# Kernel tuning notes

Measured on AMD Instinct MI355X. Metric: run time of the kernel, lower is better.

## Reference

```python
import jax, jax.numpy as jnp
import numpy as np


def setup_inputs() -> dict:
    key = jax.random.key(0)
    B, N, D = 32, 1024, 1024
    x = jax.random.normal(key, (B, N, D), dtype=jnp.float32)
    return {"x": x}


def reference(x) -> jnp.ndarray:
    # query = key = value = x (the module's Linear layers are unused).
    # kl_divs[b,i,j] = KL(softmax(x[b,i]) || softmax(x[b,j])) for i != j, 0 on diag.
    # Since KL(p||p) == 0, the full vectorized KL matrix matches the looped version.
    logp = jax.nn.log_softmax(x, axis=-1)          # [B, N, D]
    p = jnp.exp(logp)                               # softmax(x)
    neg_ent = jnp.sum(p * logp, axis=-1)            # [B, N]  = sum p log p
    cross = jnp.einsum('bid,bjd->bij', p, logp)     # [B, N, N] = sum_d p_i log q_j
    kl = neg_ent[:, :, None] - cross                # [B, N, N]
    attn = jax.nn.softmax(-kl, axis=-1)             # [B, N, N]
    out = jnp.einsum('bij,bjd->bid', attn, x)       # value = x
    return out
```

## Files before the change

### kernel.cpp

```cpp
#include <hip/hip_runtime.h>
#include <hip/hip_bf16.h>
#include <stdint.h>

#define B_ 32
#define N_ 1024
#define D_ 1024

typedef __bf16 bf16x8 __attribute__((ext_vector_type(8)));
typedef float f32x4 __attribute__((ext_vector_type(4)));

static __device__ __forceinline__ unsigned short f2bf(float f) {
    union { float f; unsigned u; } v; v.f = f;
    unsigned r = v.u + 0x7fffu + ((v.u >> 16) & 1u);
    return (unsigned short)(r >> 16);
}

static __device__ __forceinline__ void gld_lds16(const void* g, void* l) {
    __builtin_amdgcn_global_load_lds(
        (const __attribute__((address_space(1))) void*)g,
        (__attribute__((address_space(3))) void*)l, 16, 0, 0);
}

__global__ __launch_bounds__(256) void prep_kernel(const float* __restrict__ x,
        unsigned short* __restrict__ pb, unsigned short* __restrict__ xb,
        float* __restrict__ lse) {
    int row  = blockIdx.x * 4 + (threadIdx.x >> 6);
    int lane = threadIdx.x & 63;
    const float4* xr = (const float4*)(x + (size_t)row * D_);

    float4 v[4];
    #pragma unroll
    for (int q = 0; q < 4; q++) v[q] = xr[lane + 64 * q];

    float m = -1e30f;
    #pragma unroll
    for (int q = 0; q < 4; q++)
        m = fmaxf(m, fmaxf(fmaxf(v[q].x, v[q].y), fmaxf(v[q].z, v[q].w)));
    #pragma unroll
    for (int o = 1; o < 64; o <<= 1) m = fmaxf(m, __shfl_xor(m, o, 64));

    float4 e[4];
    float s = 0.0f;
    #pragma unroll
    for (int q = 0; q < 4; q++) {
        e[q].x = __expf(v[q].x - m); e[q].y = __expf(v[q].y - m);
        e[q].z = __expf(v[q].z - m); e[q].w = __expf(v[q].w - m);
        s += e[q].x + e[q].y + e[q].z + e[q].w;
    }
    #pragma unroll
    for (int o = 1; o < 64; o <<= 1) s += __shfl_xor(s, o, 64);
    float inv = 1.0f / s;

    ushort4* pr = (ushort4*)(pb + (size_t)row * D_);
    ushort4* xw = (ushort4*)(xb + (size_t)row * D_);
    #pragma unroll
    for (int q = 0; q < 4; q++) {
        ushort4 pu, xu;
        pu.x = f2bf(e[q].x * inv); pu.y = f2bf(e[q].y * inv);
        pu.z = f2bf(e[q].z * inv); pu.w = f2bf(e[q].w * inv);
        xu.x = f2bf(v[q].x); xu.y = f2bf(v[q].y);
        xu.z = f2bf(v[q].z); xu.w = f2bf(v[q].w);
        pr[lane + 64 * q] = pu;
        xw[lane + 64 * q] = xu;
    }
    if (lane == 0) lse[row] = m + logf(s);
}

template<int MODE>
__global__ __launch_bounds__(256) void gemm_bt(const unsigned short* __restrict__ Ag,
        const unsigned short* __restrict__ Bg, void* __restrict__ Cg,
        const float* __restrict__ lse, float* __restrict__ rowsum) {
    const int K = 1024;
    int b = blockIdx.z;
    const unsigned short* A  = Ag + (size_t)b * N_ * K;
    const unsigned short* Bm = Bg + (size_t)b * N_ * K;
    int m0 = blockIdx.y * 128, n0 = blockIdx.x * 128;

    __shared__ unsigned short lds[2][128 * 32];
    int t = threadIdx.x;
    int wave = t >> 6, lane = t & 63;
    int wr = wave >> 1, wc = wave & 1;

    f32x4 acc[4][4];
    #pragma unroll
    for (int i = 0; i < 4; i++)
        #pragma unroll
        for (int j = 0; j < 4; j++)
            #pragma unroll
            for (int r = 0; r < 4; r++) acc[i][j][r] = 0.0f;

    int fm = lane & 15;
    int gf = lane >> 4;

    for (int k0 = 0; k0 < K; k0 += 32) {
        __syncthreads();
        #pragma unroll
        for (int h = 0; h < 2; h++) {
            int c = h * 256 + t;
            int r = c >> 2;
            int g = (c & 3) ^ ((r >> 1) & 3);
            gld_lds16(A  + (size_t)(m0 + r) * K + k0 + g * 8, (char*)&lds[0][0] + c * 16);
            gld_lds16(Bm + (size_t)(n0 + r) * K + k0 + g * 8, (char*)&lds[1][0] + c * 16);
        }
        __syncthreads();

        bf16x8 av[4], bv[4];
        #pragma unroll
        for (int i = 0; i < 4; i++) {
            int ra = wr * 64 + i * 16 + fm;
            int rb = wc * 64 + i * 16 + fm;
            av[i] = *(const bf16x8*)&lds[0][ra * 32 + ((gf ^ ((ra >> 1) & 3)) * 8)];
            bv[i] = *(const bf16x8*)&lds[1][rb * 32 + ((gf ^ ((rb >> 1) & 3)) * 8)];
        }
        #pragma unroll
        for (int i = 0; i < 4; i++)
            #pragma unroll
            for (int j = 0; j < 4; j++)
                acc[i][j] = __builtin_amdgcn_mfma_f32_16x16x32_bf16(av[i], bv[j], acc[i][j], 0, 0, 0);
    }

    int cr = (lane >> 4) * 4;
    int cc = lane & 15;

    if (MODE == 0) {
        unsigned short* Co = (unsigned short*)Cg + (size_t)b * (size_t)N_ * N_;
        float lsev[4];
        #pragma unroll
        for (int j = 0; j < 4; j++) lsev[j] = lse[b * N_ + n0 + wc * 64 + j * 16 + cc];
        float rsum[16];
        #pragma unroll
        for (int q = 0; q < 16; q++) rsum[q] = 0.0f;
        #pragma unroll
        for (int i = 0; i < 4; i++) {
            #pragma unroll
            for (int r = 0; r < 4; r++) {
                int row = m0 + wr * 64 + i * 16 + cr + r;
                size_t ro = (size_t)row * N_;
                #pragma unroll
                for (int j = 0; j < 4; j++) {
                    int col = n0 + wc * 64 + j * 16 + cc;
                    float ev = __expf(acc[i][j][r] - lsev[j]);
                    unsigned short eb = f2bf(ev);
                    union { unsigned u; float f; } bk; bk.u = ((unsigned)eb) << 16;
                    Co[ro + col] = eb;
                    rsum[i * 4 + r] += bk.f;
                }
            }
        }
        #pragma unroll
        for (int q = 0; q < 16; q++) {
            float sv = rsum[q];
            sv += __shfl_xor(sv, 1, 64);
            sv += __shfl_xor(sv, 2, 64);
            sv += __shfl_xor(sv, 4, 64);
            sv += __shfl_xor(sv, 8, 64);
            rsum[q] = sv;
        }
        if (cc == 0) {
            #pragma unroll
            for (int q = 0; q < 16; q++) {
                int row = m0 + wr * 64 + (q >> 2) * 16 + cr + (q & 3);
                atomicAdd(&rowsum[b * N_ + row], rsum[q]);
            }
        }
    } else {
        float* Co = (float*)Cg + (size_t)b * (size_t)N_ * N_;
        #pragma unroll
        for (int i = 0; i < 4; i++) {
            #pragma unroll
            for (int r = 0; r < 4; r++) {
                int row = m0 + wr * 64 + i * 16 + cr + r;
                float inv = 1.0f / rowsum[b * N_ + row];
                size_t ro = (size_t)row * N_;
                #pragma unroll
                for (int j = 0; j < 4; j++) {
                    int col = n0 + wc * 64 + j * 16 + cc;
                    Co[ro + col] = acc[i][j][r] * inv;
                }
            }
        }
    }
}

__global__ __launch_bounds__(256) void transpose_kernel(const unsigned short* __restrict__ in,
        unsigned short* __restrict__ out) {
    int b  = blockIdx.z;
    int j0 = blockIdx.y * 64;
    int d0 = blockIdx.x * 64;
    __shared__ unsigned short tile[64][66];
    const unsigned short* ip = in + ((size_t)b * N_ + j0) * D_ + d0;
    int t = threadIdx.x;
    #pragma unroll
    for (int c = t; c < 512; c += 256) {
        int r = c >> 3, col = (c & 7) * 8;
        uint4 val = *(const uint4*)(ip + (size_t)r * D_ + col);
        unsigned int* dst = (unsigned int*)&tile[r][col];
        dst[0] = val.x; dst[1] = val.y; dst[2] = val.z; dst[3] = val.w;
    }
    __syncthreads();
    unsigned short* op = out + ((size_t)b * D_ + d0) * N_ + j0;
    #pragma unroll
    for (int c = t; c < 512; c += 256) {
        int r = c >> 3, col = (c & 7) * 8;
        unsigned short vals[8];
        #pragma unroll
        for (int k = 0; k < 8; k++) vals[k] = tile[col + k][r];
        uint4 o;
        o.x = (unsigned)vals[0] | ((unsigned)vals[1] << 16);
        o.y = (unsigned)vals[2] | ((unsigned)vals[3] << 16);
        o.z = (unsigned)vals[4] | ((unsigned)vals[5] << 16);
        o.w = (unsigned)vals[6] | ((unsigned)vals[7] << 16);
        *(uint4*)(op + (size_t)r * N_ + col) = o;
    }
}

extern "C" void kernel_launch(void* const* d_in, const int* in_sizes, int n_in,
                              void* d_out, int out_size, void* d_ws, size_t ws_size,
                              hipStream_t stream) {
    const float* x = (const float*)d_in[0];
    float* out = (float*)d_out;
    char* ws = (char*)d_ws;

    unsigned short* pb    = (unsigned short*)(ws);
    unsigned short* xb    = (unsigned short*)(ws + 67108864ULL);
    unsigned short* xbT   = (unsigned short*)(ws + 134217728ULL);
    unsigned short* attnE = (unsigned short*)(ws + 201326592ULL);
    float*          lse   = (float*)(ws + 268435456ULL);
    float*          rowsum= (float*)(ws + 268566528ULL);

    hipMemsetAsync(rowsum, 0, B_ * N_ * sizeof(float), stream);
    prep_kernel<<<dim3(B_ * N_ / 4), 256, 0, stream>>>(x, pb, xb, lse);
    transpose_kernel<<<dim3(16, 16, B_), 256, 0, stream>>>(xb, xbT);
    gemm_bt<0><<<dim3(8, 8, B_), 256, 0, stream>>>(pb, xb, attnE, lse, rowsum);
    gemm_bt<1><<<dim3(8, 8, B_), 256, 0, stream>>>(attnE, xbT, out, nullptr, rowsum);
}
```

Baseline: 480.1 us.

## Enlarge GEMM tiles to 256x256 with double-buffered async LDS pipeline

Both batched GEMMs now use 256x256 output tiles with 512 threads (8 waves, 2x4 layout). Each wave computes 128x64 in two halves. K-tiles are double-buffered in LDS, and direct global-to-LDS loads are issued up to three stages ahead, with explicit vmcnt waits, barriers and s_setprio around the MFMA blocks. The goal is more data reuse per LDS byte and loads hidden behind compute. In exchange it uses more registers and 64KB of LDS, and the grid shrinks to 512 blocks, which may lower occupancy.

```diff
diff --git a/kernel.cpp b/kernel.cpp
--- a/kernel.cpp
+++ b/kernel.cpp
@@ -67,56 +67,88 @@
 }
 
 template<int MODE>
-__global__ __launch_bounds__(256) void gemm_bt(const unsigned short* __restrict__ Ag,
+__global__ __launch_bounds__(512) void gemm_bt(const unsigned short* __restrict__ Ag,
         const unsigned short* __restrict__ Bg, void* __restrict__ Cg,
         const float* __restrict__ lse, float* __restrict__ rowsum) {
     const int K = 1024;
     int b = blockIdx.z;
     const unsigned short* A  = Ag + (size_t)b * N_ * K;
     const unsigned short* Bm = Bg + (size_t)b * N_ * K;
-    int m0 = blockIdx.y * 128, n0 = blockIdx.x * 128;
-
-    __shared__ unsigned short lds[2][128 * 32];
+    int m0 = blockIdx.y * 256, n0 = blockIdx.x * 256;
+
+    __shared__ unsigned short lds[32768];
+
     int t = threadIdx.x;
     int wave = t >> 6, lane = t & 63;
-    int wr = wave >> 1, wc = wave & 1;
-
-    f32x4 acc[4][4];
-    #pragma unroll
-    for (int i = 0; i < 4; i++)
+    int wr = wave >> 2, wc = wave & 3;
+    int fm = lane & 15, gf = lane >> 4;
+    int rsw = (fm >> 1) & 3;
+
+    f32x4 acc[8][4];
+    #pragma unroll
+    for (int i = 0; i < 8; i++)
         #pragma unroll
         for (int j = 0; j < 4; j++)
             #pragma unroll
             for (int r = 0; r < 4; r++) acc[i][j][r] = 0.0f;
 
-    int fm = lane & 15;
-    int gf = lane >> 4;
-
-    for (int k0 = 0; k0 < K; k0 += 32) {
-        __syncthreads();
-        #pragma unroll
-        for (int h = 0; h < 2; h++) {
-            int c = h * 256 + t;
-            int r = c >> 2;
-            int g = (c & 3) ^ ((r >> 1) & 3);
-            gld_lds16(A  + (size_t)(m0 + r) * K + k0 + g * 8, (char*)&lds[0][0] + c * 16);
-            gld_lds16(Bm + (size_t)(n0 + r) * K + k0 + g * 8, (char*)&lds[1][0] + c * 16);
-        }
-        __syncthreads();
-
-        bf16x8 av[4], bv[4];
-        #pragma unroll
-        for (int i = 0; i < 4; i++) {
-            int ra = wr * 64 + i * 16 + fm;
-            int rb = wc * 64 + i * 16 + fm;
-            av[i] = *(const bf16x8*)&lds[0][ra * 32 + ((gf ^ ((ra >> 1) & 3)) * 8)];
-            bv[i] = *(const bf16x8*)&lds[1][rb * 32 + ((gf ^ ((rb >> 1) & 3)) * 8)];
-        }
-        #pragma unroll
-        for (int i = 0; i < 4; i++)
-            #pragma unroll
-            for (int j = 0; j < 4; j++)
-                acc[i][j] = __builtin_amdgcn_mfma_f32_16x16x32_bf16(av[i], bv[j], acc[i][j], 0, 0, 0);
+    int rr = t >> 2, s = t & 3;
+    int sg = s ^ ((rr >> 1) & 3);
+    int rbase = rr + (rr & 64);
+
+    auto stage = [&](int g) {
+        int tg = g >> 1, qg = g & 1, bg = tg & 1;
+        int row = qg * 64 + rbase;
+        const unsigned short* sa = A  + (size_t)(m0 + row) * K + tg * 32 + sg * 8;
+        const unsigned short* sb = Bm + (size_t)(n0 + row) * K + tg * 32 + sg * 8;
+        gld_lds16(sa, &lds[bg * 8192 + row * 32 + s * 8]);
+        gld_lds16(sb, &lds[16384 + bg * 8192 + row * 32 + s * 8]);
+    };
+
+    stage(0); stage(1); stage(2);
+    asm volatile("s_waitcnt vmcnt(2)" ::: "memory");
+    __builtin_amdgcn_s_barrier();
+
+    for (int tt = 0; tt < 32; ++tt) {
+        int bb = tt & 1;
+        const unsigned short* LA = &lds[bb * 8192];
+        const unsigned short* LB = &lds[16384 + bb * 8192];
+        bf16x8 bv[4];
+        #pragma unroll
+        for (int q = 0; q < 2; ++q) {
+            if (q == 0) {
+                #pragma unroll
+                for (int j = 0; j < 4; ++j) {
+                    int row = wc * 64 + j * 16 + fm;
+                    bv[j] = *(const bf16x8*)&LB[row * 32 + (gf ^ rsw) * 8];
+                }
+            }
+            bf16x8 av[4];
+            #pragma unroll
+            for (int i2 = 0; i2 < 4; ++i2) {
+                int row = wr * 128 + (q * 4 + i2) * 16 + fm;
+                av[i2] = *(const bf16x8*)&LA[row * 32 + (gf ^ rsw) * 8];
+            }
+            int g = 2 * tt + q + 3;
+            if (g < 64) stage(g);
+
+            __builtin_amdgcn_s_barrier();
+            asm volatile("s_waitcnt lgkmcnt(0)" ::: "memory");
+            __builtin_amdgcn_sched_barrier(0);
+            __builtin_amdgcn_s_setprio(1);
+            #pragma unroll
+            for (int i2 = 0; i2 < 4; ++i2)
+                #pragma unroll
+                for (int j = 0; j < 4; ++j)
+                    acc[q * 4 + i2][j] = __builtin_amdgcn_mfma_f32_16x16x32_bf16(
+                        av[i2], bv[j], acc[q * 4 + i2][j], 0, 0, 0);
+            __builtin_amdgcn_s_setprio(0);
+            if (q == 1) {
+                if (tt < 30)       asm volatile("s_waitcnt vmcnt(2)" ::: "memory");
+                else if (tt == 30) asm volatile("s_waitcnt vmcnt(0)" ::: "memory");
+            }
+            __builtin_amdgcn_s_barrier();
+        }
     }
 
     int cr = (lane >> 4) * 4;
@@ -127,14 +159,14 @@
         float lsev[4];
         #pragma unroll
         for (int j = 0; j < 4; j++) lsev[j] = lse[b * N_ + n0 + wc * 64 + j * 16 + cc];
-        float rsum[16];
-        #pragma unroll
-        for (int q = 0; q < 16; q++) rsum[q] = 0.0f;
-        #pragma unroll
-        for (int i = 0; i < 4; i++) {
+        float rsum[32];
+        #pragma unroll
+        for (int q = 0; q < 32; q++) rsum[q] = 0.0f;
+        #pragma unroll
+        for (int i = 0; i < 8; i++) {
             #pragma unroll
             for (int r = 0; r < 4; r++) {
-                int row = m0 + wr * 64 + i * 16 + cr + r;
+                int row = m0 + wr * 128 + i * 16 + cr + r;
                 size_t ro = (size_t)row * N_;
                 #pragma unroll
                 for (int j = 0; j < 4; j++) {
@@ -148,7 +180,7 @@
             }
         }
         #pragma unroll
-        for (int q = 0; q < 16; q++) {
+        for (int q = 0; q < 32; q++) {
             float sv = rsum[q];
             sv += __shfl_xor(sv, 1, 64);
             sv += __shfl_xor(sv, 2, 64);
@@ -158,18 +190,18 @@
         }
         if (cc == 0) {
             #pragma unroll
-            for (int q = 0; q < 16; q++) {
-                int row = m0 + wr * 64 + (q >> 2) * 16 + cr + (q & 3);
+            for (int q = 0; q < 32; q++) {
+                int row = m0 + wr * 128 + (q >> 2) * 16 + cr + (q & 3);
                 atomicAdd(&rowsum[b * N_ + row], rsum[q]);
             }
         }
     } else {
         float* Co = (float*)Cg + (size_t)b * (size_t)N_ * N_;
         #pragma unroll
-        for (int i = 0; i < 4; i++) {
+        for (int i = 0; i < 8; i++) {
             #pragma unroll
             for (int r = 0; r < 4; r++) {
-                int row = m0 + wr * 64 + i * 16 + cr + r;
+                int row = m0 + wr * 128 + i * 16 + cr + r;
                 float inv = 1.0f / rowsum[b * N_ + row];
                 size_t ro = (size_t)row * N_;
                 #pragma unroll
@@ -231,6 +263,6 @@
     hipMemsetAsync(rowsum, 0, B_ * N_ * sizeof(float), stream);
     prep_kernel<<<dim3(B_ * N_ / 4), 256, 0, stream>>>(x, pb, xb, lse);
     transpose_kernel<<<dim3(16, 16, B_), 256, 0, stream>>>(xb, xbT);
-    gemm_bt<0><<<dim3(8, 8, B_), 256, 0, stream>>>(pb, xb, attnE, lse, rowsum);
-    gemm_bt<1><<<dim3(8, 8, B_), 256, 0, stream>>>(attnE, xbT, out, nullptr, rowsum);
-}
+    gemm_bt<0><<<dim3(4, 4, B_), 512, 0, stream>>>(pb, xb, attnE, lse, rowsum);
+    gemm_bt<1><<<dim3(4, 4, B_), 512, 0, stream>>>(attnE, xbT, out, nullptr, rowsum);
+}
```

New measurement: 428.0 us. -10.9%, faster.

## Rework GEMM with triple-buffered LDS pipeline, 32x32 MFMA, 256x128 tiles, block swizzle

Applied to the files above, without the earlier changes.

Rewrites the batched GEMM kernels to use 512-thread blocks with 256x128 output tiles, a three-stage LDS ring fed by async global-to-LDS loads, and explicit vmcnt waits plus raw barriers in place of per-step __syncthreads. It moves from 16x16x32 to 32x32x16 bf16 MFMA and raises wave priority during MFMA bursts. It also remaps block indices to improve L2 locality, and folds the rowsum zeroing into the prep kernel so the separate memset is gone. The aim is to hide global load latency and raise MFMA utilization, at the cost of 72KB of dynamic LDS and fragile hand-counted wait logic.

```diff
diff --git a/kernel.cpp b/kernel.cpp
--- a/kernel.cpp
+++ b/kernel.cpp
@@ -7,7 +7,7 @@
 #define D_ 1024
 
 typedef __bf16 bf16x8 __attribute__((ext_vector_type(8)));
-typedef float f32x4 __attribute__((ext_vector_type(4)));
+typedef float f32x16 __attribute__((ext_vector_type(16)));
 
 static __device__ __forceinline__ unsigned short f2bf(float f) {
     union { float f; unsigned u; } v; v.f = f;
@@ -23,7 +23,9 @@
 
 __global__ __launch_bounds__(256) void prep_kernel(const float* __restrict__ x,
         unsigned short* __restrict__ pb, unsigned short* __restrict__ xb,
-        float* __restrict__ lse) {
+        float* __restrict__ lse, float* __restrict__ rowsum) {
+    if (threadIdx.x < 4) rowsum[blockIdx.x * 4 + threadIdx.x] = 0.0f;
+
     int row  = blockIdx.x * 4 + (threadIdx.x >> 6);
     int lane = threadIdx.x & 63;
     const float4* xr = (const float4*)(x + (size_t)row * D_);
@@ -66,116 +68,159 @@
     if (lane == 0) lse[row] = m + logf(s);
 }
 
+#define VM3 asm volatile("s_waitcnt vmcnt(3)" ::: "memory")
+#define VM0 asm volatile("s_waitcnt vmcnt(0)" ::: "memory")
+#define VMN
+
+#define TILE(tt, rB, wB, DOSTAGE, VM)                                           \
+  {                                                                             \
+    bf16x8 av[2][2], bv[2][2];                                                  \
+    _Pragma("unroll") for (int kk = 0; kk < 2; ++kk) {                          \
+      _Pragma("unroll") for (int i2 = 0; i2 < 2; ++i2) av[kk][i2] = lA(rB, kk, i2); \
+      _Pragma("unroll") for (int j2 = 0; j2 < 2; ++j2) bv[kk][j2] = lB(rB, kk, j2); \
+    }                                                                           \
+    if (DOSTAGE) stage(wB, (tt) + 2);                                           \
+    asm volatile("s_waitcnt lgkmcnt(0)" ::: "memory");                          \
+    __builtin_amdgcn_s_setprio(1);                                              \
+    _Pragma("unroll") for (int kk = 0; kk < 2; ++kk)                            \
+      _Pragma("unroll") for (int i2 = 0; i2 < 2; ++i2)                          \
+        _Pragma("unroll") for (int j2 = 0; j2 < 2; ++j2)                        \
+          acc[i2][j2] = __builtin_amdgcn_mfma_f32_32x32x16_bf16(                \
+              av[kk][i2], bv[kk][j2], acc[i2][j2], 0, 0, 0);                    \
+    __builtin_amdgcn_s_setprio(0);                                              \
+    VM;                                                                         \
+    __builtin_amdgcn_s_barrier();                                               \
+  }
+
 template<int MODE>
-__global__ __launch_bounds__(256) void gemm_bt(const unsigned short* __restrict__ Ag,
+__global__ __launch_bounds__(512, 4) void gemm_bt(const unsigned short* __restrict__ Ag,
         const unsigned short* __restrict__ Bg, void* __restrict__ Cg,
         const float* __restrict__ lse, float* __restrict__ rowsum) {
     const int K = 1024;
-    int b = blockIdx.z;
+
+    int h = blockIdx.x + 8 * blockIdx.y + 32 * blockIdx.z;
+    int l = (h & 7) * 128 + (h >> 3);
+    int b  = l >> 5;
+    int m0 = ((l >> 3) & 3) * 256;
+    int n0 = (l & 7) * 128;
+
     const unsigned short* A  = Ag + (size_t)b * N_ * K;
     const unsigned short* Bm = Bg + (size_t)b * N_ * K;
-    int m0 = blockIdx.y * 128, n0 = blockIdx.x * 128;
-
-    __shared__ unsigned short lds[2][128 * 32];
+
+    extern __shared__ char lds[];
+
     int t = threadIdx.x;
     int wave = t >> 6, lane = t & 63;
-    int wr = wave >> 1, wc = wave & 1;
-
-    f32x4 acc[4][4];
-    #pragma unroll
-    for (int i = 0; i < 4; i++)
-        #pragma unroll
-        for (int j = 0; j < 4; j++)
-            #pragma unroll
-            for (int r = 0; r < 4; r++) acc[i][j][r] = 0.0f;
-
-    int fm = lane & 15;
-    int gf = lane >> 4;
-
-    for (int k0 = 0; k0 < K; k0 += 32) {
-        __syncthreads();
-        #pragma unroll
-        for (int h = 0; h < 2; h++) {
-            int c = h * 256 + t;
-            int r = c >> 2;
-            int g = (c & 3) ^ ((r >> 1) & 3);
-            gld_lds16(A  + (size_t)(m0 + r) * K + k0 + g * 8, (char*)&lds[0][0] + c * 16);
-            gld_lds16(Bm + (size_t)(n0 + r) * K + k0 + g * 8, (char*)&lds[1][0] + c * 16);
-        }
-        __syncthreads();
-
-        bf16x8 av[4], bv[4];
-        #pragma unroll
-        for (int i = 0; i < 4; i++) {
-            int ra = wr * 64 + i * 16 + fm;
-            int rb = wc * 64 + i * 16 + fm;
-            av[i] = *(const bf16x8*)&lds[0][ra * 32 + ((gf ^ ((ra >> 1) & 3)) * 8)];
-            bv[i] = *(const bf16x8*)&lds[1][rb * 32 + ((gf ^ ((rb >> 1) & 3)) * 8)];
-        }
-        #pragma unroll
-        for (int i = 0; i < 4; i++)
-            #pragma unroll
-            for (int j = 0; j < 4; j++)
-                acc[i][j] = __builtin_amdgcn_mfma_f32_16x16x32_bf16(av[i], bv[j], acc[i][j], 0, 0, 0);
-    }
-
-    int cr = (lane >> 4) * 4;
-    int cc = lane & 15;
+    int wm = wave >> 1, wn = wave & 1;
+    int ln31 = lane & 31, l5 = lane >> 5;
+
+    f32x16 acc[2][2];
+    #pragma unroll
+    for (int i = 0; i < 2; i++)
+        #pragma unroll
+        for (int j = 0; j < 2; j++)
+            #pragma unroll
+            for (int r = 0; r < 16; r++) acc[i][j][r] = 0.0f;
+
+    int rr = t >> 2, s = t & 3;
+    int sg = s ^ ((rr >> 1) & 3);
+    const unsigned short* pA0 = A  + (size_t)(m0 + rr) * K + sg * 8;
+    const unsigned short* pA1 = A  + (size_t)(m0 + 128 + rr) * K + sg * 8;
+    const unsigned short* pB0 = Bm + (size_t)(n0 + rr) * K + sg * 8;
+    int dA0 = rr * 64 + s * 16;
+    int dA1 = (128 + rr) * 64 + s * 16;
+
+    auto stage = [&](int w, int tg) {
+        char* base = lds + w * 24576;
+        gld_lds16(pA0 + tg * 32, base + dA0);
+        gld_lds16(pA1 + tg * 32, base + dA1);
+        gld_lds16(pB0 + tg * 32, base + 16384 + dA0);
+    };
+
+    auto lA = [&](int br, int kk, int i2) {
+        int row = wm * 64 + i2 * 32 + ln31;
+        int sidx = kk * 2 + l5;
+        return *(const bf16x8*)(lds + br * 24576 + row * 64 +
+                                ((sidx ^ ((row >> 1) & 3)) * 16));
+    };
+    auto lB = [&](int br, int kk, int j2) {
+        int row = wn * 64 + j2 * 32 + ln31;
+        int sidx = kk * 2 + l5;
+        return *(const bf16x8*)(lds + br * 24576 + 16384 + row * 64 +
+                                ((sidx ^ ((row >> 1) & 3)) * 16));
+    };
+
+    stage(0, 0);
+    stage(1, 1);
+    VM3;
+    __builtin_amdgcn_s_barrier();
+
+    for (int tp = 0; tp < 10; ++tp) {
+        int t0 = tp * 3;
+        TILE(t0 + 0, 0, 2, 1, VM3);
+        TILE(t0 + 1, 1, 0, 1, VM3);
+        TILE(t0 + 2, 2, 1, 1, VM3);
+    }
+    TILE(30, 0, 2, 0, VM0);
+    TILE(31, 1, 0, 0, VMN);
 
     if (MODE == 0) {
         unsigned short* Co = (unsigned short*)Cg + (size_t)b * (size_t)N_ * N_;
-        float lsev[4];
-        #pragma unroll
-        for (int j = 0; j < 4; j++) lsev[j] = lse[b * N_ + n0 + wc * 64 + j * 16 + cc];
-        float rsum[16];
-        #pragma unroll
-        for (int q = 0; q < 16; q++) rsum[q] = 0.0f;
-        #pragma unroll
-        for (int i = 0; i < 4; i++) {
-            #pragma unroll
-            for (int r = 0; r < 4; r++) {
-                int row = m0 + wr * 64 + i * 16 + cr + r;
+        float lsev[2];
+        #pragma unroll
+        for (int j2 = 0; j2 < 2; j2++)
+            lsev[j2] = lse[b * N_ + n0 + wn * 64 + j2 * 32 + ln31];
+        float rsum[2][16];
+        #pragma unroll
+        for (int i2 = 0; i2 < 2; i2++)
+            #pragma unroll
+            for (int r = 0; r < 16; r++) rsum[i2][r] = 0.0f;
+        #pragma unroll
+        for (int i2 = 0; i2 < 2; i2++) {
+            #pragma unroll
+            for (int r = 0; r < 16; r++) {
+                int row = m0 + wm * 64 + i2 * 32 + (r & 3) + 8 * (r >> 2) + 4 * l5;
                 size_t ro = (size_t)row * N_;
                 #pragma unroll
-                for (int j = 0; j < 4; j++) {
-                    int col = n0 + wc * 64 + j * 16 + cc;
-                    float ev = __expf(acc[i][j][r] - lsev[j]);
+                for (int j2 = 0; j2 < 2; j2++) {
+                    int col = n0 + wn * 64 + j2 * 32 + ln31;
+                    float ev = __expf(acc[i2][j2][r] - lsev[j2]);
                     unsigned short eb = f2bf(ev);
                     union { unsigned u; float f; } bk; bk.u = ((unsigned)eb) << 16;
                     Co[ro + col] = eb;
-                    rsum[i * 4 + r] += bk.f;
+                    rsum[i2][r] += bk.f;
                 }
             }
         }
         #pragma unroll
-        for (int q = 0; q < 16; q++) {
-            float sv = rsum[q];
-            sv += __shfl_xor(sv, 1, 64);
-            sv += __shfl_xor(sv, 2, 64);
-            sv += __shfl_xor(sv, 4, 64);
-            sv += __shfl_xor(sv, 8, 64);
-            rsum[q] = sv;
-        }
-        if (cc == 0) {
-            #pragma unroll
-            for (int q = 0; q < 16; q++) {
-                int row = m0 + wr * 64 + (q >> 2) * 16 + cr + (q & 3);
-                atomicAdd(&rowsum[b * N_ + row], rsum[q]);
+        for (int i2 = 0; i2 < 2; i2++) {
+            #pragma unroll
+            for (int r = 0; r < 16; r++) {
+                float sv = rsum[i2][r];
+                sv += __shfl_xor(sv, 1, 64);
+                sv += __shfl_xor(sv, 2, 64);
+                sv += __shfl_xor(sv, 4, 64);
+                sv += __shfl_xor(sv, 8, 64);
+                sv += __shfl_xor(sv, 16, 64);
+                if (ln31 == 0) {
+                    int row = m0 + wm * 64 + i2 * 32 + (r & 3) + 8 * (r >> 2) + 4 * l5;
+                    atomicAdd(&rowsum[b * N_ + row], sv);
+                }
             }
         }
     } else {
         float* Co = (float*)Cg + (size_t)b * (size_t)N_ * N_;
         #pragma unroll
-        for (int i = 0; i < 4; i++) {
-            #pragma unroll
-            for (int r = 0; r < 4; r++) {
-                int row = m0 + wr * 64 + i * 16 + cr + r;
+        for (int i2 = 0; i2 < 2; i2++) {
+            #pragma unroll
+            for (int r = 0; r < 16; r++) {
+                int row = m0 + wm * 64 + i2 * 32 + (r & 3) + 8 * (r >> 2) + 4 * l5;
                 float inv = 1.0f / rowsum[b * N_ + row];
                 size_t ro = (size_t)row * N_;
                 #pragma unroll
-                for (int j = 0; j < 4; j++) {
-                    int col = n0 + wc * 64 + j * 16 + cc;
-                    Co[ro + col] = acc[i][j][r] * inv;
+                for (int j2 = 0; j2 < 2; j2++) {
+                    int col = n0 + wn * 64 + j2 * 32 + ln31;
+                    Co[ro + col] = acc[i2][j2][r] * inv;
                 }
             }
         }
@@ -228,9 +273,8 @@
     float*          lse   = (float*)(ws + 268435456ULL);
     float*          rowsum= (float*)(ws + 268566528ULL);
 
-    hipMemsetAsync(rowsum, 0, B_ * N_ * sizeof(float), stream);
-    prep_kernel<<<dim3(B_ * N_ / 4), 256, 0, stream>>>(x, pb, xb, lse);
+    prep_kernel<<<dim3(B_ * N_ / 4), 256, 0, stream>>>(x, pb, xb, lse, rowsum);
     transpose_kernel<<<dim3(16, 16, B_), 256, 0, stream>>>(xb, xbT);
-    gemm_bt<0><<<dim3(8, 8, B_), 256, 0, stream>>>(pb, xb, attnE, lse, rowsum);
-    gemm_bt<1><<<dim3(8, 8, B_), 256, 0, stream>>>(attnE, xbT, out, nullptr, rowsum);
-}
+    gemm_bt<0><<<dim3(8, 4, B_), 512, 73728, stream>>>(pb, xb, attnE, lse, rowsum);
+    gemm_bt<1><<<dim3(8, 4, B_), 512, 73728, stream>>>(attnE, xbT, out, nullptr, rowsum);
+}
```

Measured after the change: 462.2 us. -3.7%, faster.
